# Kernel optimization log

Measured on AMD Instinct MI355X. Metric: run time of the kernel, lower is better.

## Reference

```python
import jax, jax.numpy as jnp
import numpy as np
from jax import lax

B, T, IN, H = 4096, 512, 11, 16


def lstm(x, Wih, Whh, bih, bhh):
    # x: [B, T, in]; PyTorch gate order i, f, g, o packed along 4H.
    xg = jnp.einsum('bti,gi->btg', x, Wih) + bih + bhh  # [B, T, 4H]
    h0 = jnp.zeros((x.shape[0], Whh.shape[1]), x.dtype)
    c0 = jnp.zeros_like(h0)

    def step(carry, xg_t):
        h, c = carry
        g = xg_t + h @ Whh.T                      # [B, 4H]
        i, f, gg, o = jnp.split(g, 4, axis=-1)
        i = jax.nn.sigmoid(i)
        f = jax.nn.sigmoid(f)
        gg = jnp.tanh(gg)
        o = jax.nn.sigmoid(o)
        c = f * c + i * gg
        h = o * jnp.tanh(c)
        return (h, c), h

    _, hs = lax.scan(step, (h0, c0), jnp.swapaxes(xg, 0, 1))  # hs: [T, B, H]
    return jnp.swapaxes(hs, 0, 1)  # [B, T, H]


def setup_inputs() -> dict:
    key = jax.random.key(0)
    ks = jax.random.split(key, 16)
    s = 1.0 / np.sqrt(H)
    u = lambda k, shape: jax.random.uniform(k, shape, jnp.float32, -s, s)
    return {
        'x': jax.random.normal(ks[0], (B, T, IN), jnp.float32),
        'Wih1': u(ks[1], (4 * H, IN)), 'Whh1': u(ks[2], (4 * H, H)),
        'bih1': u(ks[3], (4 * H,)), 'bhh1': u(ks[4], (4 * H,)),
        'Wih2': u(ks[5], (4 * H, H)), 'Whh2': u(ks[6], (4 * H, H)),
        'bih2': u(ks[7], (4 * H,)), 'bhh2': u(ks[8], (4 * H,)),
        'Wd1': u(ks[9], (8, H)), 'bd1': u(ks[10], (8,)),
        'Wd2': u(ks[11], (8, 8)), 'bd2': u(ks[12], (8,)),
        'Wd3': u(ks[13], (3, 8)), 'bd3': u(ks[14], (3,)),
    }


def reference(x, Wih1, Whh1, bih1, bhh1, Wih2, Whh2, bih2, bhh2,
              Wd1, bd1, Wd2, bd2, Wd3, bd3):
    h1 = lstm(x, Wih1, Whh1, bih1, bhh1)          # [B, T, H]
    # Dropout2d treated as identity (eval mode).
    h2 = lstm(h1, Wih2, Whh2, bih2, bhh2)          # [B, T, H]
    s = jax.nn.softmax(h2, axis=1)[:, -1, :]       # softmax over TIME, take last step -> [B, H]
    d = (s @ Wd1.T + bd1) @ Wd2.T + bd2
    d = d @ Wd3.T + bd3                            # [B, 3]
    return jax.nn.softmax(d, axis=1)
```

## Files before the change

### kernel.cpp

```cpp
#include <hip/hip_runtime.h>

#define T_STEPS 512
#define IN_DIM 11
#define ROW_PAD 12
#define H_DIM 16
#define ROW_F (T_STEPS * IN_DIM)
#define CHUNK_T 16
#define CHUNK_F (CHUNK_T * IN_DIM)
#define N_CHUNK (T_STEPS / CHUNK_T)
#define NB 2
#define LOG2E 1.44269504088896340736f

typedef float v2f __attribute__((ext_vector_type(2)));
typedef float v4f __attribute__((ext_vector_type(4)));

__device__ __forceinline__ v2f pk_fma(v2f a, v2f b, v2f c) {
    v2f d;
    asm("v_pk_fma_f32 %0, %1, %2, %3" : "=v"(d) : "v"(a), "v"(b), "v"(c));
    return d;
}

template<int CTRL>
__device__ __forceinline__ float qperm(float v) {
    return __builtin_bit_cast(float,
        __builtin_amdgcn_update_dpp(0, __builtin_bit_cast(int, v),
                                    CTRL, 0xf, 0xf, true));
}

__device__ __forceinline__ float bcast_lane(float v, int l) {
    return __builtin_bit_cast(float,
        __builtin_amdgcn_readlane(__builtin_bit_cast(int, v), l));
}

#define ACT_STEP(gsum, cst, hv_out)                                           \
    {                                                                         \
        const float a_ = __builtin_fmaf(vAa,                                  \
            __builtin_amdgcn_rcpf(1.0f + __builtin_amdgcn_exp2f(gsum)), vBc); \
        const float gi_ = qperm<0x00>(a_);                                    \
        const float gf_ = qperm<0x55>(a_);                                    \
        const float gg_ = qperm<0xAA>(a_);                                    \
        const float go_ = qperm<0xFF>(a_);                                    \
        cst = __builtin_fmaf(gf_, cst, gi_ * gg_);                            \
        const float tc_ = __builtin_fmaf(2.0f,                                \
            __builtin_amdgcn_rcpf(1.0f +                                      \
                __builtin_amdgcn_exp2f(-2.0f * LOG2E * cst)), -1.0f);         \
        hv_out = go_ * tc_;                                                   \
    }

__global__ __launch_bounds__(256, 2) void lstm2_head(
    const float* __restrict__ x,
    const float* __restrict__ Wih1, const float* __restrict__ Whh1,
    const float* __restrict__ bih1, const float* __restrict__ bhh1,
    const float* __restrict__ Wih2, const float* __restrict__ Whh2,
    const float* __restrict__ bih2, const float* __restrict__ bhh2,
    const float* __restrict__ Wd1, const float* __restrict__ bd1,
    const float* __restrict__ Wd2, const float* __restrict__ bd2,
    const float* __restrict__ Wd3, const float* __restrict__ bd3,
    float* __restrict__ out)
{
    __shared__ alignas(16) float xlds[4][NB][2][212];
    __shared__ alignas(16) float shh[4][NB][2][H_DIM];

    const int lane = threadIdx.x & 63;
    const int wid = __builtin_amdgcn_readfirstlane((int)(threadIdx.x >> 6));
    const int b0 = blockIdx.x * (4 * NB) + wid * NB;

    const int r   = lane >> 2;
    const int gt  = lane & 3;
    const int row = gt * H_DIM + r;

    const bool is_t = (gt == 2);
    const float M   = is_t ? (-2.0f * LOG2E) : (-LOG2E);
    const float vAa = is_t ? 2.0f : 1.0f;
    const float vBc = is_t ? -1.0f : 0.0f;

    v2f wi1p[6], wh1p[8], wi2p[8], wh2p[8];
    #pragma unroll
    for (int j = 0; j < 5; ++j)
        wi1p[j] = (v2f){M * Wih1[row * IN_DIM + 2 * j], M * Wih1[row * IN_DIM + 2 * j + 1]};
    wi1p[5] = (v2f){M * Wih1[row * IN_DIM + 10], 0.0f};
    #pragma unroll
    for (int j = 0; j < 8; ++j) {
        wh1p[j] = (v2f){M * Whh1[row * H_DIM + 2 * j], M * Whh1[row * H_DIM + 2 * j + 1]};
        wi2p[j] = (v2f){M * Wih2[row * H_DIM + 2 * j], M * Wih2[row * H_DIM + 2 * j + 1]};
        wh2p[j] = (v2f){M * Whh2[row * H_DIM + 2 * j], M * Whh2[row * H_DIM + 2 * j + 1]};
    }
    const float bb1 = M * (bih1[row] + bhh1[row]);
    const float bb2 = M * (bih2[row] + bhh2[row]);
    #pragma unroll
    for (int j = 0; j < 6; ++j) asm volatile("" : "+v"(wi1p[j]));
    #pragma unroll
    for (int j = 0; j < 8; ++j) {
        asm volatile("" : "+v"(wh1p[j]));
        asm volatile("" : "+v"(wi2p[j]));
        asm volatile("" : "+v"(wh2p[j]));
    }

    const float* __restrict__ xb[NB];
    #pragma unroll
    for (int bi = 0; bi < NB; ++bi) xb[bi] = x + (size_t)(b0 + bi) * ROW_F;

    float* hs1[NB]; float* hs2[NB];
    const v4f* h1q4[NB]; const v4f* h2q4[NB];
    #pragma unroll
    for (int bi = 0; bi < NB; ++bi) {
        hs1[bi] = &shh[wid][bi][0][0];
        hs2[bi] = &shh[wid][bi][1][0];
        h1q4[bi] = (const v4f*)hs1[bi];
        h2q4[bi] = (const v4f*)hs2[bi];
    }

    if (lane < 32) {
        const int buf = lane >> 4, rr = lane & 15;
        xlds[wid][0][buf][rr * ROW_PAD + IN_DIM] = 0.0f;
        xlds[wid][1][buf][rr * ROW_PAD + IN_DIM] = 0.0f;
    }

    const int f1i = lane, f2i = lane + 64, f3i = lane + 128;
    const int p1 = (f1i / IN_DIM) * ROW_PAD + (f1i % IN_DIM);
    const int p2 = (f2i / IN_DIM) * ROW_PAD + (f2i % IN_DIM);
    const int p3 = (f3i / IN_DIM) * ROW_PAD + (f3i % IN_DIM);

    float gl0[NB], gl1[NB], gl2[NB];
    #pragma unroll
    for (int bi = 0; bi < NB; ++bi) {
        gl0[bi] = xb[bi][f1i];
        gl1[bi] = xb[bi][f2i];
        gl2[bi] = xb[bi][min(f3i, ROW_F - 1)];
    }

    float c1[NB], c2[NB], h2v[NB], ssum[NB];
    v2f h1r[NB][8], h2r[NB][8];
    #pragma unroll
    for (int bi = 0; bi < NB; ++bi) {
        c1[bi] = 0.f; c2[bi] = 0.f; h2v[bi] = 0.f; ssum[bi] = 0.f;
        #pragma unroll
        for (int j = 0; j < 8; ++j) {
            h1r[bi][j] = (v2f){0.f, 0.f};
            h2r[bi][j] = (v2f){0.f, 0.f};
        }
    }

    for (int ck = 0; ck < N_CHUNK; ++ck) {
        float* xbuf[NB];
        #pragma unroll
        for (int bi = 0; bi < NB; ++bi) {
            xbuf[bi] = &xlds[wid][bi][ck & 1][0];
            xbuf[bi][p1] = gl0[bi];
            xbuf[bi][p2] = gl1[bi];
            xbuf[bi][p3] = gl2[bi];
        }
        if (ck + 1 < N_CHUNK) {
            const int base = (ck + 1) * CHUNK_F;
            #pragma unroll
            for (int bi = 0; bi < NB; ++bi) {
                gl0[bi] = xb[bi][base + f1i];
                gl1[bi] = xb[bi][base + f2i];
                gl2[bi] = xb[bi][min(base + f3i, ROW_F - 1)];
            }
        }

        #pragma unroll
        for (int t2 = 0; t2 < CHUNK_T; ++t2) {
            v2f a2p[NB], a2q[NB], a1p[NB], a1q[NB];

            #pragma unroll
            for (int bi = 0; bi < NB; ++bi) {
                a2p[bi] = pk_fma(wh2p[0], h2r[bi][0], (v2f){bb2, 0.f});
                a2q[bi] = pk_fma(wh2p[1], h2r[bi][1], (v2f){0.f, 0.f});
                #pragma unroll
                for (int j = 2; j < 8; j += 2) {
                    a2p[bi] = pk_fma(wh2p[j],     h2r[bi][j],     a2p[bi]);
                    a2q[bi] = pk_fma(wh2p[j + 1], h2r[bi][j + 1], a2q[bi]);
                }
            }

            #pragma unroll
            for (int bi = 0; bi < NB; ++bi) {
                const v2f* const xr = (const v2f*)(xbuf[bi] + t2 * ROW_PAD);
                a1p[bi] = pk_fma(wi1p[0], xr[0], (v2f){bb1, 0.f});
                a1q[bi] = pk_fma(wi1p[1], xr[1], (v2f){0.f, 0.f});
                #pragma unroll
                for (int j = 2; j < 6; j += 2) {
                    a1p[bi] = pk_fma(wi1p[j],     xr[j],     a1p[bi]);
                    a1q[bi] = pk_fma(wi1p[j + 1], xr[j + 1], a1q[bi]);
                }
                #pragma unroll
                for (int j = 0; j < 8; j += 2) {
                    a1p[bi] = pk_fma(wh1p[j],     h1r[bi][j],     a1p[bi]);
                    a1q[bi] = pk_fma(wh1p[j + 1], h1r[bi][j + 1], a1q[bi]);
                }
            }

            float h1v[NB];
            #pragma unroll
            for (int bi = 0; bi < NB; ++bi) {
                const v2f s1 = a1p[bi] + a1q[bi];
                const float g1 = s1.x + s1.y;
                ACT_STEP(g1, c1[bi], h1v[bi]);
                hs1[bi][r] = h1v[bi];
            }
            #pragma unroll
            for (int bi = 0; bi < NB; ++bi) {
                #pragma unroll
                for (int j = 0; j < 4; ++j) {
                    const v4f q = h1q4[bi][j];
                    h1r[bi][2 * j]     = (v2f){q.x, q.y};
                    h1r[bi][2 * j + 1] = (v2f){q.z, q.w};
                }
            }

            #pragma unroll
            for (int bi = 0; bi < NB; ++bi) {
                #pragma unroll
                for (int j = 0; j < 8; j += 2) {
                    a2p[bi] = pk_fma(wi2p[j],     h1r[bi][j],     a2p[bi]);
                    a2q[bi] = pk_fma(wi2p[j + 1], h1r[bi][j + 1], a2q[bi]);
                }
            }

            #pragma unroll
            for (int bi = 0; bi < NB; ++bi) {
                const v2f s2 = a2p[bi] + a2q[bi];
                const float g2 = s2.x + s2.y;
                ACT_STEP(g2, c2[bi], h2v[bi]);
                hs2[bi][r] = h2v[bi];
            }
            #pragma unroll
            for (int bi = 0; bi < NB; ++bi) {
                #pragma unroll
                for (int j = 0; j < 4; ++j) {
                    const v4f q = h2q4[bi][j];
                    h2r[bi][2 * j]     = (v2f){q.x, q.y};
                    h2r[bi][2 * j + 1] = (v2f){q.z, q.w};
                }
                ssum[bi] += __builtin_amdgcn_exp2f(LOG2E * h2v[bi]);
            }
        }
    }

    #pragma unroll
    for (int bi = 0; bi < NB; ++bi) {
        const int b = b0 + bi;
        const float sv = __builtin_amdgcn_exp2f(LOG2E * h2v[bi]) / ssum[bi];

        float ssb[H_DIM];
        #pragma unroll
        for (int k = 0; k < H_DIM; ++k) ssb[k] = bcast_lane(sv, 4 * k);

        const int r8 = lane & 7;
        float acc1 = bd1[r8];
        #pragma unroll
        for (int k = 0; k < H_DIM; ++k)
            acc1 = __builtin_fmaf(Wd1[r8 * H_DIM + k], ssb[k], acc1);

        float d1s[8];
        #pragma unroll
        for (int j = 0; j < 8; ++j) d1s[j] = bcast_lane(acc1, j);

        float acc2 = bd2[r8];
        #pragma unroll
        for (int k = 0; k < 8; ++k)
            acc2 = __builtin_fmaf(Wd2[r8 * 8 + k], d1s[k], acc2);

        float d2s[8];
        #pragma unroll
        for (int j = 0; j < 8; ++j) d2s[j] = bcast_lane(acc2, j);

        float lg = 0.f;
        if (lane < 3) {
            lg = bd3[lane];
            #pragma unroll
            for (int k = 0; k < 8; ++k)
                lg = __builtin_fmaf(Wd3[lane * 8 + k], d2s[k], lg);
        }
        const float l0 = bcast_lane(lg, 0);
        const float l1 = bcast_lane(lg, 1);
        const float l2 = bcast_lane(lg, 2);
        const float mx = fmaxf(l0, fmaxf(l1, l2));
        const float e0 = __builtin_amdgcn_exp2f(LOG2E * (l0 - mx));
        const float e1 = __builtin_amdgcn_exp2f(LOG2E * (l1 - mx));
        const float e2 = __builtin_amdgcn_exp2f(LOG2E * (l2 - mx));
        const float inv = 1.0f / (e0 + e1 + e2);
        if (lane < 3) {
            const float ev = (lane == 0) ? e0 : ((lane == 1) ? e1 : e2);
            out[b * 3 + lane] = ev * inv;
        }
    }
}

extern "C" void kernel_launch(void* const* d_in, const int* in_sizes, int n_in,
                              void* d_out, int out_size, void* d_ws, size_t ws_size,
                              hipStream_t stream) {
    (void)in_sizes; (void)n_in; (void)out_size; (void)d_ws; (void)ws_size;
    const float* x    = (const float*)d_in[0];
    const float* Wih1 = (const float*)d_in[1];
    const float* Whh1 = (const float*)d_in[2];
    const float* bih1 = (const float*)d_in[3];
    const float* bhh1 = (const float*)d_in[4];
    const float* Wih2 = (const float*)d_in[5];
    const float* Whh2 = (const float*)d_in[6];
    const float* bih2 = (const float*)d_in[7];
    const float* bhh2 = (const float*)d_in[8];
    const float* Wd1  = (const float*)d_in[9];
    const float* bd1  = (const float*)d_in[10];
    const float* Wd2  = (const float*)d_in[11];
    const float* bd2  = (const float*)d_in[12];
    const float* Wd3  = (const float*)d_in[13];
    const float* bd3  = (const float*)d_in[14];

    lstm2_head<<<dim3(4096 / (4 * NB)), dim3(256), 0, stream>>>(
        x, Wih1, Whh1, bih1, bhh1, Wih2, Whh2, bih2, bhh2,
        Wd1, bd1, Wd2, bd2, Wd3, bd3, (float*)d_out);
}
```

Measured before the change: 499.3 us.

## Split gate dot products across lane quads and reduce with DPP quad permutes

Each lane in a quad of four now holds a 4-wide slice of the input/hidden dimension for all four gates, not the full 16-wide row for its own gate. The partial sums are exchanged with quad permutes and added, so each lane ends up with its own gate's pre-activation. This cuts the per-lane FMA count and the LDS reads per step (one float4 instead of four), at the cost of extra cross-lane permutes and adds. The x staging rows are padded to 16 so each lane can do a single aligned vector load.

```diff
diff --git a/kernel.cpp b/kernel.cpp
--- a/kernel.cpp
+++ b/kernel.cpp
@@ -2,7 +2,7 @@
 
 #define T_STEPS 512
 #define IN_DIM 11
-#define ROW_PAD 12
+#define ROW_PAD 16
 #define H_DIM 16
 #define ROW_F (T_STEPS * IN_DIM)
 #define CHUNK_T 16
@@ -58,7 +58,7 @@
     const float* __restrict__ Wd3, const float* __restrict__ bd3,
     float* __restrict__ out)
 {
-    __shared__ alignas(16) float xlds[4][NB][2][212];
+    __shared__ alignas(16) float xlds[4][NB][2][CHUNK_T * ROW_PAD];
     __shared__ alignas(16) float shh[4][NB][2][H_DIM];
 
     const int lane = threadIdx.x & 63;
@@ -70,76 +70,87 @@
     const int row = gt * H_DIM + r;
 
     const bool is_t = (gt == 2);
-    const float M   = is_t ? (-2.0f * LOG2E) : (-LOG2E);
     const float vAa = is_t ? 2.0f : 1.0f;
     const float vBc = is_t ? -1.0f : 0.0f;
-
-    v2f wi1p[6], wh1p[8], wi2p[8], wh2p[8];
-    #pragma unroll
-    for (int j = 0; j < 5; ++j)
-        wi1p[j] = (v2f){M * Wih1[row * IN_DIM + 2 * j], M * Wih1[row * IN_DIM + 2 * j + 1]};
-    wi1p[5] = (v2f){M * Wih1[row * IN_DIM + 10], 0.0f};
-    #pragma unroll
-    for (int j = 0; j < 8; ++j) {
-        wh1p[j] = (v2f){M * Whh1[row * H_DIM + 2 * j], M * Whh1[row * H_DIM + 2 * j + 1]};
-        wi2p[j] = (v2f){M * Wih2[row * H_DIM + 2 * j], M * Wih2[row * H_DIM + 2 * j + 1]};
-        wh2p[j] = (v2f){M * Whh2[row * H_DIM + 2 * j], M * Whh2[row * H_DIM + 2 * j + 1]};
-    }
-    const float bb1 = M * (bih1[row] + bhh1[row]);
-    const float bb2 = M * (bih2[row] + bhh2[row]);
-    #pragma unroll
-    for (int j = 0; j < 6; ++j) asm volatile("" : "+v"(wi1p[j]));
-    #pragma unroll
-    for (int j = 0; j < 8; ++j) {
-        asm volatile("" : "+v"(wh1p[j]));
-        asm volatile("" : "+v"(wi2p[j]));
-        asm volatile("" : "+v"(wh2p[j]));
+    const float Mown = is_t ? (-2.0f * LOG2E) : (-LOG2E);
+
+    v2f w1h[4][2], w1x[4][2], w2h[4][2], w2i[4][2];
+    #pragma unroll
+    for (int j = 0; j < 4; ++j) {
+        const int gj = gt ^ j;
+        const float Mj = (gj == 2) ? (-2.0f * LOG2E) : (-LOG2E);
+        const int rowj = gj * H_DIM + r;
+        #pragma unroll
+        for (int i2 = 0; i2 < 2; ++i2) {
+            const int k0 = 4 * gt + 2 * i2, k1 = k0 + 1;
+            w1h[j][i2] = (v2f){Mj * Whh1[rowj * H_DIM + k0],
+                               Mj * Whh1[rowj * H_DIM + k1]};
+            w1x[j][i2] = (v2f){k0 < IN_DIM ? Mj * Wih1[rowj * IN_DIM + k0] : 0.f,
+                               k1 < IN_DIM ? Mj * Wih1[rowj * IN_DIM + k1] : 0.f};
+            w2h[j][i2] = (v2f){Mj * Whh2[rowj * H_DIM + k0],
+                               Mj * Whh2[rowj * H_DIM + k1]};
+            w2i[j][i2] = (v2f){Mj * Wih2[rowj * H_DIM + k0],
+                               Mj * Wih2[rowj * H_DIM + k1]};
+        }
+    }
+    const float bb1 = Mown * (bih1[row] + bhh1[row]);
+    const float bb2 = Mown * (bih2[row] + bhh2[row]);
+    #pragma unroll
+    for (int j = 0; j < 4; ++j) {
+        #pragma unroll
+        for (int i2 = 0; i2 < 2; ++i2) {
+            asm volatile("" : "+v"(w1h[j][i2]));
+            asm volatile("" : "+v"(w1x[j][i2]));
+            asm volatile("" : "+v"(w2h[j][i2]));
+            asm volatile("" : "+v"(w2i[j][i2]));
+        }
     }
 
     const float* __restrict__ xb[NB];
-    #pragma unroll
-    for (int bi = 0; bi < NB; ++bi) xb[bi] = x + (size_t)(b0 + bi) * ROW_F;
-
-    float* hs1[NB]; float* hs2[NB];
-    const v4f* h1q4[NB]; const v4f* h2q4[NB];
+    float* hsl1[NB]; float* hsl2[NB];
     #pragma unroll
     for (int bi = 0; bi < NB; ++bi) {
-        hs1[bi] = &shh[wid][bi][0][0];
-        hs2[bi] = &shh[wid][bi][1][0];
-        h1q4[bi] = (const v4f*)hs1[bi];
-        h2q4[bi] = (const v4f*)hs2[bi];
-    }
-
-    if (lane < 32) {
-        const int buf = lane >> 4, rr = lane & 15;
-        xlds[wid][0][buf][rr * ROW_PAD + IN_DIM] = 0.0f;
-        xlds[wid][1][buf][rr * ROW_PAD + IN_DIM] = 0.0f;
-    }
-
-    const int f1i = lane, f2i = lane + 64, f3i = lane + 128;
+        xb[bi] = x + (size_t)(b0 + bi) * ROW_F;
+        hsl1[bi] = &shh[wid][bi][0][0];
+        hsl2[bi] = &shh[wid][bi][1][0];
+    }
+
+    #pragma unroll
+    for (int idx = 0; idx < CHUNK_T * ROW_PAD; idx += 64) {
+        const int s = idx + lane;
+        if ((s & 15) >= IN_DIM) {
+            #pragma unroll
+            for (int bi = 0; bi < NB; ++bi) {
+                xlds[wid][bi][0][s] = 0.f;
+                xlds[wid][bi][1][s] = 0.f;
+            }
+        }
+    }
+
+    const int f1i = lane, f2i = lane + 64;
+    const int f3c = min(lane + 128, CHUNK_F - 1);
     const int p1 = (f1i / IN_DIM) * ROW_PAD + (f1i % IN_DIM);
     const int p2 = (f2i / IN_DIM) * ROW_PAD + (f2i % IN_DIM);
-    const int p3 = (f3i / IN_DIM) * ROW_PAD + (f3i % IN_DIM);
+    const int p3 = (f3c / IN_DIM) * ROW_PAD + (f3c % IN_DIM);
 
     float gl0[NB], gl1[NB], gl2[NB];
     #pragma unroll
     for (int bi = 0; bi < NB; ++bi) {
         gl0[bi] = xb[bi][f1i];
         gl1[bi] = xb[bi][f2i];
-        gl2[bi] = xb[bi][min(f3i, ROW_F - 1)];
+        gl2[bi] = xb[bi][f3c];
     }
 
     float c1[NB], c2[NB], h2v[NB], ssum[NB];
-    v2f h1r[NB][8], h2r[NB][8];
+    v2f h1a[NB], h1b[NB], h2a[NB], h2b[NB];
     #pragma unroll
     for (int bi = 0; bi < NB; ++bi) {
         c1[bi] = 0.f; c2[bi] = 0.f; h2v[bi] = 0.f; ssum[bi] = 0.f;
-        #pragma unroll
-        for (int j = 0; j < 8; ++j) {
-            h1r[bi][j] = (v2f){0.f, 0.f};
-            h2r[bi][j] = (v2f){0.f, 0.f};
-        }
-    }
+        h1a[bi] = (v2f){0.f, 0.f}; h1b[bi] = (v2f){0.f, 0.f};
+        h2a[bi] = (v2f){0.f, 0.f}; h2b[bi] = (v2f){0.f, 0.f};
+    }
+
+    const int xoff = 4 * gt;
 
     for (int ck = 0; ck < N_CHUNK; ++ck) {
         float* xbuf[NB];
@@ -156,84 +167,94 @@
             for (int bi = 0; bi < NB; ++bi) {
                 gl0[bi] = xb[bi][base + f1i];
                 gl1[bi] = xb[bi][base + f2i];
-                gl2[bi] = xb[bi][min(base + f3i, ROW_F - 1)];
+                gl2[bi] = xb[bi][base + f3c];
             }
         }
 
         #pragma unroll
         for (int t2 = 0; t2 < CHUNK_T; ++t2) {
-            v2f a2p[NB], a2q[NB], a1p[NB], a1q[NB];
-
-            #pragma unroll
-            for (int bi = 0; bi < NB; ++bi) {
-                a2p[bi] = pk_fma(wh2p[0], h2r[bi][0], (v2f){bb2, 0.f});
-                a2q[bi] = pk_fma(wh2p[1], h2r[bi][1], (v2f){0.f, 0.f});
-                #pragma unroll
-                for (int j = 2; j < 8; j += 2) {
-                    a2p[bi] = pk_fma(wh2p[j],     h2r[bi][j],     a2p[bi]);
-                    a2q[bi] = pk_fma(wh2p[j + 1], h2r[bi][j + 1], a2q[bi]);
-                }
-            }
-
-            #pragma unroll
-            for (int bi = 0; bi < NB; ++bi) {
-                const v2f* const xr = (const v2f*)(xbuf[bi] + t2 * ROW_PAD);
-                a1p[bi] = pk_fma(wi1p[0], xr[0], (v2f){bb1, 0.f});
-                a1q[bi] = pk_fma(wi1p[1], xr[1], (v2f){0.f, 0.f});
-                #pragma unroll
-                for (int j = 2; j < 6; j += 2) {
-                    a1p[bi] = pk_fma(wi1p[j],     xr[j],     a1p[bi]);
-                    a1q[bi] = pk_fma(wi1p[j + 1], xr[j + 1], a1q[bi]);
-                }
-                #pragma unroll
-                for (int j = 0; j < 8; j += 2) {
-                    a1p[bi] = pk_fma(wh1p[j],     h1r[bi][j],     a1p[bi]);
-                    a1q[bi] = pk_fma(wh1p[j + 1], h1r[bi][j + 1], a1q[bi]);
-                }
-            }
-
-            float h1v[NB];
-            #pragma unroll
-            for (int bi = 0; bi < NB; ++bi) {
-                const v2f s1 = a1p[bi] + a1q[bi];
-                const float g1 = s1.x + s1.y;
-                ACT_STEP(g1, c1[bi], h1v[bi]);
-                hs1[bi][r] = h1v[bi];
-            }
-            #pragma unroll
-            for (int bi = 0; bi < NB; ++bi) {
-                #pragma unroll
-                for (int j = 0; j < 4; ++j) {
-                    const v4f q = h1q4[bi][j];
-                    h1r[bi][2 * j]     = (v2f){q.x, q.y};
-                    h1r[bi][2 * j + 1] = (v2f){q.z, q.w};
-                }
-            }
-
-            #pragma unroll
-            for (int bi = 0; bi < NB; ++bi) {
-                #pragma unroll
-                for (int j = 0; j < 8; j += 2) {
-                    a2p[bi] = pk_fma(wi2p[j],     h1r[bi][j],     a2p[bi]);
-                    a2q[bi] = pk_fma(wi2p[j + 1], h1r[bi][j + 1], a2q[bi]);
-                }
-            }
-
-            #pragma unroll
-            for (int bi = 0; bi < NB; ++bi) {
-                const v2f s2 = a2p[bi] + a2q[bi];
-                const float g2 = s2.x + s2.y;
-                ACT_STEP(g2, c2[bi], h2v[bi]);
-                hs2[bi][r] = h2v[bi];
-            }
-            #pragma unroll
-            for (int bi = 0; bi < NB; ++bi) {
-                #pragma unroll
-                for (int j = 0; j < 4; ++j) {
-                    const v4f q = h2q4[bi][j];
-                    h2r[bi][2 * j]     = (v2f){q.x, q.y};
-                    h2r[bi][2 * j + 1] = (v2f){q.z, q.w};
-                }
+            v2f e0[NB], e1[NB], e2[NB], e3[NB];
+            #pragma unroll
+            for (int bi = 0; bi < NB; ++bi) {
+                e0[bi] = pk_fma(w2h[0][0], h2a[bi], (v2f){bb2, 0.f});
+                e0[bi] = pk_fma(w2h[0][1], h2b[bi], e0[bi]);
+                e1[bi] = pk_fma(w2h[1][0], h2a[bi], (v2f){0.f, 0.f});
+                e1[bi] = pk_fma(w2h[1][1], h2b[bi], e1[bi]);
+                e2[bi] = pk_fma(w2h[2][0], h2a[bi], (v2f){0.f, 0.f});
+                e2[bi] = pk_fma(w2h[2][1], h2b[bi], e2[bi]);
+                e3[bi] = pk_fma(w2h[3][0], h2a[bi], (v2f){0.f, 0.f});
+                e3[bi] = pk_fma(w2h[3][1], h2b[bi], e3[bi]);
+            }
+
+            float g1v[NB];
+            #pragma unroll
+            for (int bi = 0; bi < NB; ++bi) {
+                const v4f xq = *(const v4f*)(xbuf[bi] + t2 * ROW_PAD + xoff);
+                const v2f x01 = (v2f){xq.x, xq.y};
+                const v2f x23 = (v2f){xq.z, xq.w};
+                v2f d0 = pk_fma(w1h[0][0], h1a[bi], (v2f){bb1, 0.f});
+                d0 = pk_fma(w1h[0][1], h1b[bi], d0);
+                d0 = pk_fma(w1x[0][0], x01, d0);
+                d0 = pk_fma(w1x[0][1], x23, d0);
+                v2f d1 = pk_fma(w1h[1][0], h1a[bi], (v2f){0.f, 0.f});
+                d1 = pk_fma(w1h[1][1], h1b[bi], d1);
+                d1 = pk_fma(w1x[1][0], x01, d1);
+                d1 = pk_fma(w1x[1][1], x23, d1);
+                v2f d2 = pk_fma(w1h[2][0], h1a[bi], (v2f){0.f, 0.f});
+                d2 = pk_fma(w1h[2][1], h1b[bi], d2);
+                d2 = pk_fma(w1x[2][0], x01, d2);
+                d2 = pk_fma(w1x[2][1], x23, d2);
+                v2f d3 = pk_fma(w1h[3][0], h1a[bi], (v2f){0.f, 0.f});
+                d3 = pk_fma(w1h[3][1], h1b[bi], d3);
+                d3 = pk_fma(w1x[3][0], x01, d3);
+                d3 = pk_fma(w1x[3][1], x23, d3);
+                const float u0 = d0.x + d0.y;
+                const float u1 = d1.x + d1.y;
+                const float u2 = d2.x + d2.y;
+                const float u3 = d3.x + d3.y;
+                g1v[bi] = u0 + qperm<0xB1>(u1) + qperm<0x4E>(u2) + qperm<0x1B>(u3);
+            }
+
+            #pragma unroll
+            for (int bi = 0; bi < NB; ++bi) {
+                float h1v;
+                ACT_STEP(g1v[bi], c1[bi], h1v);
+                hsl1[bi][r] = h1v;
+            }
+            #pragma unroll
+            for (int bi = 0; bi < NB; ++bi) {
+                const v4f h1q = *(const v4f*)(hsl1[bi] + xoff);
+                h1a[bi] = (v2f){h1q.x, h1q.y};
+                h1b[bi] = (v2f){h1q.z, h1q.w};
+            }
+
+            float g2v[NB];
+            #pragma unroll
+            for (int bi = 0; bi < NB; ++bi) {
+                e0[bi] = pk_fma(w2i[0][0], h1a[bi], e0[bi]);
+                e0[bi] = pk_fma(w2i[0][1], h1b[bi], e0[bi]);
+                e1[bi] = pk_fma(w2i[1][0], h1a[bi], e1[bi]);
+                e1[bi] = pk_fma(w2i[1][1], h1b[bi], e1[bi]);
+                e2[bi] = pk_fma(w2i[2][0], h1a[bi], e2[bi]);
+                e2[bi] = pk_fma(w2i[2][1], h1b[bi], e2[bi]);
+                e3[bi] = pk_fma(w2i[3][0], h1a[bi], e3[bi]);
+                e3[bi] = pk_fma(w2i[3][1], h1b[bi], e3[bi]);
+                const float v0 = e0[bi].x + e0[bi].y;
+                const float v1 = e1[bi].x + e1[bi].y;
+                const float v2 = e2[bi].x + e2[bi].y;
+                const float v3 = e3[bi].x + e3[bi].y;
+                g2v[bi] = v0 + qperm<0xB1>(v1) + qperm<0x4E>(v2) + qperm<0x1B>(v3);
+            }
+            #pragma unroll
+            for (int bi = 0; bi < NB; ++bi) {
+                ACT_STEP(g2v[bi], c2[bi], h2v[bi]);
+                hsl2[bi][r] = h2v[bi];
+            }
+            #pragma unroll
+            for (int bi = 0; bi < NB; ++bi) {
+                const v4f h2q = *(const v4f*)(hsl2[bi] + xoff);
+                h2a[bi] = (v2f){h2q.x, h2q.y};
+                h2b[bi] = (v2f){h2q.z, h2q.w};
                 ssum[bi] += __builtin_amdgcn_exp2f(LOG2E * h2v[bi]);
             }
         }
```

After: 492.0 us. Within noise of the previous version (-1.5%).
